# Kernel optimization log

Measured on AMD Instinct MI355X. Metric: run time of the kernel, lower is better.

The kernel has to match this reference:

```python
import jax, jax.numpy as jnp
import numpy as np

D_MODEL = 1024
N_HEADS = 16
D_K = D_MODEL // N_HEADS
D_FF = 4096
B, S = 2, 2048
LN_EPS = 1e-5
NEG_INF = -1e30  # finite stand-in for -inf; first (all-masked) row is overwritten by zeros anyway


def layer_norm(x, g, b):
    mu = jnp.mean(x, axis=-1, keepdims=True)
    var = jnp.mean(jnp.square(x - mu), axis=-1, keepdims=True)
    return (x - mu) * jax.lax.rsqrt(var + LN_EPS) * g + b


def setup_inputs() -> dict:
    key = jax.random.key(0)
    ks = jax.random.split(key, 16)
    sd = 0.02
    inp = {
        "query": jax.random.normal(ks[0], (B, S, D_MODEL), jnp.float32),
        "key": jax.random.normal(ks[1], (B, S, D_MODEL), jnp.float32),
        "values": jax.random.normal(ks[2], (B, S, D_MODEL), jnp.float32),
        "Wq": jax.random.normal(ks[3], (D_MODEL, D_MODEL), jnp.float32) * sd,
        "bq": jnp.zeros((D_MODEL,), jnp.float32),
        "Wk": jax.random.normal(ks[4], (D_MODEL, D_MODEL), jnp.float32) * sd,
        "bk": jnp.zeros((D_MODEL,), jnp.float32),
        "Wv": jax.random.normal(ks[5], (D_MODEL, D_MODEL), jnp.float32) * sd,
        "bv": jnp.zeros((D_MODEL,), jnp.float32),
        "Wo": jax.random.normal(ks[6], (D_MODEL, D_MODEL), jnp.float32) * sd,
        "bo": jnp.zeros((D_MODEL,), jnp.float32),
        "ln1_g": jnp.ones((D_MODEL,), jnp.float32),
        "ln1_b": jnp.zeros((D_MODEL,), jnp.float32),
        "W1": jax.random.normal(ks[7], (D_MODEL, D_FF), jnp.float32) * sd,
        "b1": jnp.zeros((D_FF,), jnp.float32),
        "W2": jax.random.normal(ks[8], (D_FF, D_MODEL), jnp.float32) * sd,
        "b2": jnp.zeros((D_MODEL,), jnp.float32),
        "ln2_g": jnp.ones((D_MODEL,), jnp.float32),
        "ln2_b": jnp.zeros((D_MODEL,), jnp.float32),
        "mask": 0,
    }
    return inp


def reference(query, key, values, Wq, bq, Wk, bk, Wv, bv, Wo, bo,
              ln1_g, ln1_b, W1, b1, W2, b2, ln2_g, ln2_b, mask):
    b, s, d = query.shape
    # projections -> [B, H, S, d_k]
    q = (query @ Wq + bq).reshape(b, s, N_HEADS, D_K).transpose(0, 2, 1, 3)
    k = (key @ Wk + bk).reshape(b, s, N_HEADS, D_K).transpose(0, 2, 1, 3)
    v = (values @ Wv + bv).reshape(b, s, N_HEADS, D_K).transpose(0, 2, 1, 3)
    # scores [B, H, S, S]
    scores = jnp.einsum("bhqd,bhkd->bhqk", q, k) / jnp.sqrt(jnp.float32(D_K))
    # torch: triu(ones, k=mask)==0 -> allowed iff j < i + mask
    i = jnp.arange(s)[:, None]
    j = jnp.arange(s)[None, :]
    allowed = j < (i + mask)
    scores = jnp.where(allowed, scores, NEG_INF)
    attn = jax.nn.softmax(scores, axis=-1)
    if mask == 0:
        # zero-pad trick: first query row (fully masked) is replaced by zeros
        attn = attn.at[:, :, 0, :].set(0.0)
    ctx = jnp.einsum("bhqk,bhkd->bhqd", attn, v)
    ctx = ctx.transpose(0, 2, 1, 3).reshape(b, s, d)
    attn_out = ctx @ Wo + bo
    x = layer_norm(query + attn_out, ln1_g, ln1_b)
    ffn = jax.nn.relu(x @ W1 + b1) @ W2 + b2
    out = layer_norm(x + ffn, ln2_g, ln2_b)
    return out
```

## Files before the change

### kernel.cpp

```cpp
#include <hip/hip_runtime.h>


typedef __attribute__((ext_vector_type(8))) __bf16 bf16x8;
typedef __attribute__((ext_vector_type(4))) float f32x4;

struct alignas(8)  S4 { short x, y, z, w; };
struct alignas(16) F4 { float x, y, z, w; };
struct alignas(16) I4 { int x, y, z, w; };

static __device__ __forceinline__ short f2bf(float f) {
  unsigned u = __float_as_uint(f);
  u += 0x7fff + ((u >> 16) & 1);
  return (short)(u >> 16);
}

static __device__ __forceinline__ void store_out(float* p, float v) { *p = v; }
static __device__ __forceinline__ void store_out(short* p, float v) { *p = f2bf(v); }

#define GLL16(g, l)                                                         \
  __builtin_amdgcn_global_load_lds(                                         \
      (__attribute__((address_space(1))) void*)(g),                         \
      (__attribute__((address_space(3))) void*)(l), 16, 0, 0)

__global__ __launch_bounds__(256) void cvt_bf16_kernel(
    const float* __restrict__ i0, const float* __restrict__ i1,
    const float* __restrict__ i2, short* __restrict__ o0,
    short* __restrict__ o1, short* __restrict__ o2) {
  int z = blockIdx.y;
  const float* in = z == 0 ? i0 : (z == 1 ? i1 : i2);
  short* out = z == 0 ? o0 : (z == 1 ? o1 : o2);
  int i = (blockIdx.x * 256 + threadIdx.x) * 4;
  F4 v = *(const F4*)(in + i);
  S4 o = { f2bf(v.x), f2bf(v.y), f2bf(v.z), f2bf(v.w) };
  *(S4*)(out + i) = o;
}

__global__ __launch_bounds__(256) void transpose_cvt_kernel(
    const float* __restrict__ Wq, const float* __restrict__ Wk,
    const float* __restrict__ Wv, const float* __restrict__ Wo,
    const float* __restrict__ W1, const float* __restrict__ W2,
    short* __restrict__ Wqt, short* __restrict__ Wkt,
    short* __restrict__ Wvt, short* __restrict__ Wot,
    short* __restrict__ W1t, short* __restrict__ W2t) {
  __shared__ float tile[64][65];
  int bid = blockIdx.x;
  const float* W; short* Wt; int K, N, kx, ny;
  if (bid < 1024) {
    int w = bid >> 8, t = bid & 255;
    W = w == 0 ? Wq : (w == 1 ? Wk : (w == 2 ? Wv : Wo));
    Wt = w == 0 ? Wqt : (w == 1 ? Wkt : (w == 2 ? Wvt : Wot));
    K = 1024; N = 1024; kx = t & 15; ny = t >> 4;
  } else if (bid < 2048) {
    int t = bid - 1024;
    W = W1; Wt = W1t; K = 1024; N = 4096; kx = t & 15; ny = t >> 4;
  } else {
    int t = bid - 2048;
    W = W2; Wt = W2t; K = 4096; N = 1024; kx = t & 63; ny = t >> 6;
  }
  int k0 = kx * 64, n0 = ny * 64;
  int tid = threadIdx.x;
  int rr = tid >> 4, cc = (tid & 15) * 4;
#pragma unroll
  for (int p = 0; p < 4; ++p) {
    int row = p * 16 + rr;
    F4 v = *(const F4*)&W[(long)(k0 + row) * N + n0 + cc];
    tile[row][cc] = v.x; tile[row][cc + 1] = v.y;
    tile[row][cc + 2] = v.z; tile[row][cc + 3] = v.w;
  }
  __syncthreads();
#pragma unroll
  for (int p = 0; p < 4; ++p) {
    int rn = p * 16 + rr;
    S4 o = { f2bf(tile[cc + 0][rn]), f2bf(tile[cc + 1][rn]),
             f2bf(tile[cc + 2][rn]), f2bf(tile[cc + 3][rn]) };
    *(S4*)&Wt[(long)(n0 + rn) * K + k0 + cc] = o;
  }
}

template <int OUT_MODE, bool RELU, bool RES, typename OT>
__device__ __forceinline__ void gemm_core(
    const short* __restrict__ A, const short* __restrict__ Bt,
    const float* __restrict__ bias, const float* __restrict__ res,
    OT* __restrict__ out, int M, int N, int K) {
  __shared__ __align__(16) short sA[128 * 64];
  __shared__ __align__(16) short sB[128 * 64];
  int tid = threadIdx.x;
  int lane = tid & 63, wave = tid >> 6;
  int col = lane & 15, quad = lane >> 4;
  int m0 = blockIdx.x * 128, n0 = blockIdx.y * 128;
  int wm = (wave & 1) * 64, wn = (wave >> 1) * 64;

  f32x4 acc[4][4] = {};

  for (int k0 = 0; k0 < K; k0 += 64) {
    __syncthreads();
#pragma unroll
    for (int j = 0; j < 4; ++j) {
      int idx = j * 256 + tid;
      int row = idx >> 3, cp = idx & 7;
      int c = cp ^ (row & 7);
      const short* ga = A  + (long)(m0 + row) * K + k0 + c * 8;
      const short* gb = Bt + (long)(n0 + row) * K + k0 + c * 8;
      short* la = &sA[(j * 256 + (wave << 6)) * 8];
      short* lb = &sB[(j * 256 + (wave << 6)) * 8];
      GLL16(ga, la);
      GLL16(gb, lb);
    }
    __syncthreads();

#pragma unroll
    for (int kk = 0; kk < 2; ++kk) {
      bf16x8 a[4], b[4];
#pragma unroll
      for (int t = 0; t < 4; ++t) {
        int ra = wm + t * 16 + col;
        int ca = kk * 4 + quad;
        a[t] = *(const bf16x8*)&sA[ra * 64 + ((ca ^ (ra & 7)) << 3)];
        int rb = wn + t * 16 + col;
        b[t] = *(const bf16x8*)&sB[rb * 64 + ((ca ^ (rb & 7)) << 3)];
      }
#pragma unroll
      for (int t = 0; t < 4; ++t)
#pragma unroll
        for (int u = 0; u < 4; ++u)
          acc[t][u] = __builtin_amdgcn_mfma_f32_16x16x32_bf16(
              a[t], b[u], acc[t][u], 0, 0, 0);
    }
  }

#pragma unroll
  for (int t = 0; t < 4; ++t) {
#pragma unroll
    for (int u = 0; u < 4; ++u) {
      int Cc = n0 + wn + u * 16 + col;
      float bv = bias[Cc];
#pragma unroll
      for (int r = 0; r < 4; ++r) {
        int R = m0 + wm + t * 16 + quad * 4 + r;
        float v = acc[t][u][r] + bv;
        if (RES) v += res[(long)R * N + Cc];
        if (RELU) v = v > 0.f ? v : 0.f;
        if (OUT_MODE == 0) {
          store_out(&out[(long)R * N + Cc], v);
        } else {
          int bb = R >> 11, s = R & 2047, h = Cc >> 6, d = Cc & 63;
          store_out(&out[((long)((bb * 16 + h) * 2048 + s) << 6) + d], v);
        }
      }
    }
  }
}

template <int OUT_MODE, bool RELU, bool RES, typename OT>
__global__ __launch_bounds__(256) void gemm_bt(
    const short* __restrict__ A, const short* __restrict__ Bt,
    const float* __restrict__ bias, const float* __restrict__ res,
    OT* __restrict__ out, int M, int N, int K) {
  gemm_core<OUT_MODE, RELU, RES, OT>(A, Bt, bias, res, out, M, N, K);
}

__global__ __launch_bounds__(256) void gemm_qkv(
    const short* __restrict__ Aq, const short* __restrict__ Ak,
    const short* __restrict__ Av, const short* __restrict__ Btq,
    const short* __restrict__ Btk, const short* __restrict__ Btv,
    const float* __restrict__ bq, const float* __restrict__ bk,
    const float* __restrict__ bv, short* __restrict__ Qp,
    short* __restrict__ Kp, short* __restrict__ Vp) {
  int z = blockIdx.z;
  const short* A = z == 0 ? Aq : (z == 1 ? Ak : Av);
  const short* Bt = z == 0 ? Btq : (z == 1 ? Btk : Btv);
  const float* bias = z == 0 ? bq : (z == 1 ? bk : bv);
  short* out = z == 0 ? Qp : (z == 1 ? Kp : Vp);
  gemm_core<1, false, false, short>(A, Bt, bias, nullptr, out, 4096, 1024, 1024);
}

__global__ __launch_bounds__(256) void attn_kernel(
    const short* __restrict__ Q, const short* __restrict__ K,
    const short* __restrict__ V, const int* __restrict__ maskp,
    short* __restrict__ ctx) {
  __shared__ __align__(16) short sK[2][64 * 64];
  __shared__ __align__(16) int   sVt[2][64 * 32];
  __shared__ __align__(16) short sP[4 * 16 * 64];
  int tid = threadIdx.x, lane = tid & 63, wave = tid >> 6;
  int col = lane & 15, quad = lane >> 4;
  int pair = blockIdx.x, bh = blockIdx.y;
  int maskv = maskp[0];
  const long base = (long)bh * (2048 * 64);
  int b = bh >> 4, h = bh & 15;

  int kp = tid & 31, dg = tid >> 5, d0v = dg * 8;

  for (int pass = 0; pass < 2; ++pass) {
    int qt = pass ? (31 - pair) : pair;
    int i0 = qt * 64 + wave * 16;

    long jmax = (long)qt * 64 + 63 + maskv - 1;
    int tot = (jmax < 0) ? 0 : (int)(jmax >> 6) + 1;
    if (tot > 32) tot = 32;

    bf16x8 aQ[2];
#pragma unroll
    for (int kk = 0; kk < 2; ++kk)
      aQ[kk] = *(const bf16x8*)&Q[base + (long)(i0 + col) * 64 + kk * 32 + quad * 8];

    f32x4 o[4] = {};
    float lsum[4] = { 0.f, 0.f, 0.f, 0.f };

    if (tot > 0) {
#pragma unroll
      for (int j = 0; j < 2; ++j) {
        int idx = j * 256 + tid;
        int row = idx >> 3, cp = idx & 7;
        int c = cp ^ (row & 7);
        GLL16(K + base + (long)row * 64 + c * 8,
              &sK[0][(j * 256 + (wave << 6)) * 8]);
      }
      {
        union { I4 v; short s[8]; } u0, u1;
        u0.v = *(const I4*)&V[base + (long)(2 * kp) * 64 + d0v];
        u1.v = *(const I4*)&V[base + (long)(2 * kp + 1) * 64 + d0v];
#pragma unroll
        for (int j = 0; j < 8; ++j) {
          int d = d0v + j;
          int w = ((int)(unsigned short)u1.s[j] << 16) | (unsigned short)u0.s[j];
          sVt[0][d * 32 + ((((kp >> 2) ^ (d & 7)) << 2) | (kp & 3))] = w;
        }
      }
    }
    __syncthreads();

    for (int kt = 0; kt < tot; ++kt) {
      int cur = kt & 1, nxt = cur ^ 1;
      bool pf = (kt + 1 < tot);

      union { I4 v; short s[8]; } u0, u1;
      if (pf) {
#pragma unroll
        for (int j = 0; j < 2; ++j) {
          int idx = j * 256 + tid;
          int row = idx >> 3, cp = idx & 7;
          int c = cp ^ (row & 7);
          GLL16(K + base + (long)((kt + 1) * 64 + row) * 64 + c * 8,
                &sK[nxt][(j * 256 + (wave << 6)) * 8]);
        }
        u0.v = *(const I4*)&V[base + (long)((kt + 1) * 64 + 2 * kp) * 64 + d0v];
        u1.v = *(const I4*)&V[base + (long)((kt + 1) * 64 + 2 * kp + 1) * 64 + d0v];
      }

      f32x4 sc[4] = {};
#pragma unroll
      for (int kk = 0; kk < 2; ++kk) {
        int ca = kk * 4 + quad;
#pragma unroll
        for (int nt = 0; nt < 4; ++nt) {
          int rk = nt * 16 + col;
          bf16x8 bK = *(const bf16x8*)&sK[cur][rk * 64 + ((ca ^ (rk & 7)) << 3)];
          sc[nt] = __builtin_amdgcn_mfma_f32_16x16x32_bf16(aQ[kk], bK, sc[nt], 0, 0, 0);
        }
      }

      bool interior = (kt * 64 + 63) < (qt * 64 + maskv);
      if (interior) {
#pragma unroll
        for (int r = 0; r < 4; ++r) {
          int qr = quad * 4 + r;
#pragma unroll
          for (int nt = 0; nt < 4; ++nt) {
            float p = __expf(sc[nt][r] * 0.125f);
            lsum[r] += p;
            int k8 = nt * 2 + (col >> 3);
            sP[wave * 1024 + qr * 64 + (((k8 ^ (qr & 7)) << 3) | (col & 7))] =
                f2bf(p);
          }
        }
      } else {
#pragma unroll
        for (int r = 0; r < 4; ++r) {
          int i = i0 + quad * 4 + r;
          int qr = quad * 4 + r;
#pragma unroll
          for (int nt = 0; nt < 4; ++nt) {
            int j = kt * 64 + nt * 16 + col;
            float p = (j < i + maskv) ? __expf(sc[nt][r] * 0.125f) : 0.f;
            lsum[r] += p;
            int k8 = nt * 2 + (col >> 3);
            sP[wave * 1024 + qr * 64 + (((k8 ^ (qr & 7)) << 3) | (col & 7))] =
                f2bf(p);
          }
        }
      }

#pragma unroll
      for (int kk = 0; kk < 2; ++kk) {
        int ca = kk * 4 + quad;
        bf16x8 aP = *(const bf16x8*)&sP[wave * 1024 + col * 64 + ((ca ^ (col & 7)) << 3)];
#pragma unroll
        for (int dt = 0; dt < 4; ++dt) {
          int d = dt * 16 + col;
          bf16x8 bV = *(const bf16x8*)((const short*)sVt[cur] + d * 64 + ((ca ^ (d & 7)) << 3));
          o[dt] = __builtin_amdgcn_mfma_f32_16x16x32_bf16(aP, bV, o[dt], 0, 0, 0);
        }
      }

      if (pf) {
#pragma unroll
        for (int j = 0; j < 8; ++j) {
          int d = d0v + j;
          int w = ((int)(unsigned short)u1.s[j] << 16) | (unsigned short)u0.s[j];
          sVt[nxt][d * 32 + ((((kp >> 2) ^ (d & 7)) << 2) | (kp & 3))] = w;
        }
      }
      __syncthreads();
    }

#pragma unroll
    for (int r = 0; r < 4; ++r)
#pragma unroll
      for (int off = 1; off < 16; off <<= 1)
        lsum[r] += __shfl_xor(lsum[r], off);

#pragma unroll
    for (int r = 0; r < 4; ++r) {
      int i = i0 + quad * 4 + r;
      float inv = (lsum[r] > 0.f) ? 1.f / lsum[r] : 0.f;
      if (maskv == 0 && i == 0) inv = 0.f;
#pragma unroll
      for (int dt = 0; dt < 4; ++dt)
        ctx[(long)(b * 2048 + i) * 1024 + h * 64 + dt * 16 + col] =
            f2bf(o[dt][r] * inv);
    }
    __syncthreads();
  }
}

__global__ __launch_bounds__(256) void ln_kernel(
    const float* __restrict__ in, const float* __restrict__ g,
    const float* __restrict__ b, float* __restrict__ outf,
    short* __restrict__ outb) {
  int r = blockIdx.x, tid = threadIdx.x;
  int lane = tid & 63, wave = tid >> 6;
  F4 v = ((const F4*)(in + (long)r * 1024))[tid];
  float s = v.x + v.y + v.z + v.w;
  float sq = v.x * v.x + v.y * v.y + v.z * v.z + v.w * v.w;
#pragma unroll
  for (int off = 1; off < 64; off <<= 1) {
    s += __shfl_xor(s, off);
    sq += __shfl_xor(sq, off);
  }
  __shared__ float rs[4], rq[4];
  if (lane == 0) { rs[wave] = s; rq[wave] = sq; }
  __syncthreads();
  s = rs[0] + rs[1] + rs[2] + rs[3];
  sq = rq[0] + rq[1] + rq[2] + rq[3];
  float mu = s * (1.0f / 1024.0f);
  float var = sq * (1.0f / 1024.0f) - mu * mu;
  float rstd = rsqrtf(var + 1e-5f);
  F4 gv = ((const F4*)g)[tid], bv = ((const F4*)b)[tid];
  F4 o;
  o.x = (v.x - mu) * rstd * gv.x + bv.x;
  o.y = (v.y - mu) * rstd * gv.y + bv.y;
  o.z = (v.z - mu) * rstd * gv.z + bv.z;
  o.w = (v.w - mu) * rstd * gv.w + bv.w;
  ((F4*)(outf + (long)r * 1024))[tid] = o;
  if (outb) {
    S4 ob = { f2bf(o.x), f2bf(o.y), f2bf(o.z), f2bf(o.w) };
    ((S4*)(outb + (long)r * 1024))[tid] = ob;
  }
}

extern "C" void kernel_launch(void* const* d_in, const int* in_sizes, int n_in,
                              void* d_out, int out_size, void* d_ws, size_t ws_size,
                              hipStream_t stream) {
  const float* query  = (const float*)d_in[0];
  const float* keyi   = (const float*)d_in[1];
  const float* values = (const float*)d_in[2];
  const float* Wq = (const float*)d_in[3];
  const float* bq = (const float*)d_in[4];
  const float* Wk = (const float*)d_in[5];
  const float* bk = (const float*)d_in[6];
  const float* Wv = (const float*)d_in[7];
  const float* bv = (const float*)d_in[8];
  const float* Wo = (const float*)d_in[9];
  const float* bo = (const float*)d_in[10];
  const float* ln1_g = (const float*)d_in[11];
  const float* ln1_b = (const float*)d_in[12];
  const float* W1 = (const float*)d_in[13];
  const float* b1 = (const float*)d_in[14];
  const float* W2 = (const float*)d_in[15];
  const float* b2 = (const float*)d_in[16];
  const float* ln2_g = (const float*)d_in[17];
  const float* ln2_b = (const float*)d_in[18];
  const int*   maskp = (const int*)d_in[19];
  float* out = (float*)d_out;

  char* ws = (char*)d_ws;
  const size_t MB = 1u << 20;
  short* q_bf = (short*)(ws + 0);
  short* k_bf = (short*)(ws + 8 * MB);
  short* v_bf = (short*)(ws + 16 * MB);
  short* ctx  = (short*)(ws + 24 * MB);
  short* Qp   = (short*)(ws + 32 * MB);
  short* Kp   = (short*)(ws + 40 * MB);
  short* Vp   = (short*)(ws + 48 * MB);
  float* attn_res = (float*)(ws + 0);
  float* ffn_res  = (float*)(ws + 16 * MB);
  float* x_f32    = (float*)(ws + 32 * MB);
  short* x_bf     = (short*)(ws + 48 * MB);
  short* Wqt = (short*)(ws + 56 * MB);
  short* Wkt = (short*)(ws + 58 * MB);
  short* Wvt = (short*)(ws + 60 * MB);
  short* Wot = (short*)(ws + 62 * MB);
  short* W1t = (short*)(ws + 64 * MB);
  short* W2t = (short*)(ws + 72 * MB);
  short* hbuf = (short*)(ws + 80 * MB);

  cvt_bf16_kernel<<<dim3(4096, 3), 256, 0, stream>>>(query, keyi, values,
                                                     q_bf, k_bf, v_bf);
  transpose_cvt_kernel<<<3072, 256, 0, stream>>>(Wq, Wk, Wv, Wo, W1, W2,
                                                 Wqt, Wkt, Wvt, Wot, W1t, W2t);
  gemm_qkv<<<dim3(32, 8, 3), 256, 0, stream>>>(q_bf, k_bf, v_bf,
                                               Wqt, Wkt, Wvt,
                                               bq, bk, bv, Qp, Kp, Vp);
  attn_kernel<<<dim3(16, 32), 256, 0, stream>>>(Qp, Kp, Vp, maskp, ctx);
  gemm_bt<0, false, true, float><<<dim3(32, 8), 256, 0, stream>>>(
      ctx, Wot, bo, query, attn_res, 4096, 1024, 1024);
  ln_kernel<<<4096, 256, 0, stream>>>(attn_res, ln1_g, ln1_b, x_f32, x_bf);
  gemm_bt<0, true, false, short><<<dim3(32, 32), 256, 0, stream>>>(
      x_bf, W1t, b1, nullptr, hbuf, 4096, 4096, 1024);
  gemm_bt<0, false, true, float><<<dim3(32, 8), 256, 0, stream>>>(
      hbuf, W2t, b2, x_f32, ffn_res, 4096, 1024, 4096);
  ln_kernel<<<4096, 256, 0, stream>>>(ffn_res, ln2_g, ln2_b, out, nullptr);

  (void)in_sizes; (void)n_in; (void)out_size; (void)ws_size;
}
```

Before: 422.9 us.

## Split-K the N=1024 GEMMs and fold partial sums into LayerNorm

The Wo and W2 projections, whose output is 4096x1024, now run as two-way split-K GEMMs. Each half writes fp32 partials to its own buffer, which doubles the grid from 256 to 512 blocks so the many compute units on the chip are better occupied. The residual add moves out of the GEMM epilogue into a new LayerNorm kernel that sums both partials plus the residual before normalising. The cost is extra fp32 partial traffic to and from memory, and each split block has half as many K iterations to amortise its epilogue.

```diff
diff --git a/kernel.cpp b/kernel.cpp
--- a/kernel.cpp
+++ b/kernel.cpp
@@ -81,7 +81,7 @@
 __device__ __forceinline__ void gemm_core(
     const short* __restrict__ A, const short* __restrict__ Bt,
     const float* __restrict__ bias, const float* __restrict__ res,
-    OT* __restrict__ out, int M, int N, int K) {
+    OT* __restrict__ out, int M, int N, int K, int kBeg, int kEnd) {
   __shared__ __align__(16) short sA[128 * 64];
   __shared__ __align__(16) short sB[128 * 64];
   int tid = threadIdx.x;
@@ -92,7 +92,7 @@
 
   f32x4 acc[4][4] = {};
 
-  for (int k0 = 0; k0 < K; k0 += 64) {
+  for (int k0 = kBeg; k0 < kEnd; k0 += 64) {
     __syncthreads();
 #pragma unroll
     for (int j = 0; j < 4; ++j) {
@@ -133,7 +133,7 @@
 #pragma unroll
     for (int u = 0; u < 4; ++u) {
       int Cc = n0 + wn + u * 16 + col;
-      float bv = bias[Cc];
+      float bv = bias ? bias[Cc] : 0.f;
 #pragma unroll
       for (int r = 0; r < 4; ++r) {
         int R = m0 + wm + t * 16 + quad * 4 + r;
@@ -156,7 +156,19 @@
     const short* __restrict__ A, const short* __restrict__ Bt,
     const float* __restrict__ bias, const float* __restrict__ res,
     OT* __restrict__ out, int M, int N, int K) {
-  gemm_core<OUT_MODE, RELU, RES, OT>(A, Bt, bias, res, out, M, N, K);
+  gemm_core<OUT_MODE, RELU, RES, OT>(A, Bt, bias, res, out, M, N, K, 0, K);
+}
+
+__global__ __launch_bounds__(256) void gemm_splitk(
+    const short* __restrict__ A, const short* __restrict__ Bt,
+    const float* __restrict__ bias, float* __restrict__ p0,
+    float* __restrict__ p1, int M, int N, int K) {
+  int z = blockIdx.z;
+  float* out = z == 0 ? p0 : p1;
+  const float* b = z == 0 ? bias : nullptr;
+  int kc = K >> 1;
+  gemm_core<0, false, false, float>(A, Bt, b, nullptr, out, M, N, K,
+                                    z * kc, z * kc + kc);
 }
 
 __global__ __launch_bounds__(256) void gemm_qkv(
@@ -171,7 +183,8 @@
   const short* Bt = z == 0 ? Btq : (z == 1 ? Btk : Btv);
   const float* bias = z == 0 ? bq : (z == 1 ? bk : bv);
   short* out = z == 0 ? Qp : (z == 1 ? Kp : Vp);
-  gemm_core<1, false, false, short>(A, Bt, bias, nullptr, out, 4096, 1024, 1024);
+  gemm_core<1, false, false, short>(A, Bt, bias, nullptr, out,
+                                    4096, 1024, 1024, 0, 1024);
 }
 
 __global__ __launch_bounds__(256) void attn_kernel(
@@ -333,13 +346,18 @@
   }
 }
 
-__global__ __launch_bounds__(256) void ln_kernel(
-    const float* __restrict__ in, const float* __restrict__ g,
+__global__ __launch_bounds__(256) void ln_comb_kernel(
+    const float* __restrict__ p0, const float* __restrict__ p1,
+    const float* __restrict__ res, const float* __restrict__ g,
     const float* __restrict__ b, float* __restrict__ outf,
     short* __restrict__ outb) {
   int r = blockIdx.x, tid = threadIdx.x;
   int lane = tid & 63, wave = tid >> 6;
-  F4 v = ((const F4*)(in + (long)r * 1024))[tid];
+  long off0 = (long)r * 1024;
+  F4 a = ((const F4*)(p0 + off0))[tid];
+  F4 c = ((const F4*)(p1 + off0))[tid];
+  F4 d = ((const F4*)(res + off0))[tid];
+  F4 v = { a.x + c.x + d.x, a.y + c.y + d.y, a.z + c.z + d.z, a.w + c.w + d.w };
   float s = v.x + v.y + v.z + v.w;
   float sq = v.x * v.x + v.y * v.y + v.z * v.z + v.w * v.w;
 #pragma unroll
@@ -361,10 +379,10 @@
   o.y = (v.y - mu) * rstd * gv.y + bv.y;
   o.z = (v.z - mu) * rstd * gv.z + bv.z;
   o.w = (v.w - mu) * rstd * gv.w + bv.w;
-  ((F4*)(outf + (long)r * 1024))[tid] = o;
+  ((F4*)(outf + off0))[tid] = o;
   if (outb) {
     S4 ob = { f2bf(o.x), f2bf(o.y), f2bf(o.z), f2bf(o.w) };
-    ((S4*)(outb + (long)r * 1024))[tid] = ob;
+    ((S4*)(outb + off0))[tid] = ob;
   }
 }
 
@@ -402,17 +420,19 @@
   short* Qp   = (short*)(ws + 32 * MB);
   short* Kp   = (short*)(ws + 40 * MB);
   short* Vp   = (short*)(ws + 48 * MB);
-  float* attn_res = (float*)(ws + 0);
-  float* ffn_res  = (float*)(ws + 16 * MB);
-  float* x_f32    = (float*)(ws + 32 * MB);
-  short* x_bf     = (short*)(ws + 48 * MB);
-  short* Wqt = (short*)(ws + 56 * MB);
-  short* Wkt = (short*)(ws + 58 * MB);
-  short* Wvt = (short*)(ws + 60 * MB);
-  short* Wot = (short*)(ws + 62 * MB);
-  short* W1t = (short*)(ws + 64 * MB);
-  short* W2t = (short*)(ws + 72 * MB);
+  short* Wqt  = (short*)(ws + 56 * MB);
+  short* Wkt  = (short*)(ws + 58 * MB);
+  short* Wvt  = (short*)(ws + 60 * MB);
+  short* Wot  = (short*)(ws + 62 * MB);
+  short* W1t  = (short*)(ws + 64 * MB);
+  short* W2t  = (short*)(ws + 72 * MB);
   short* hbuf = (short*)(ws + 80 * MB);
+  float* pWo0 = (float*)(ws + 0);
+  float* pWo1 = (float*)(ws + 32 * MB);
+  float* x_f32 = (float*)(ws + 16 * MB);
+  short* x_bf  = (short*)(ws + 48 * MB);
+  float* pF0 = (float*)(ws + 0);
+  float* pF1 = (float*)(ws + 32 * MB);
 
   cvt_bf16_kernel<<<dim3(4096, 3), 256, 0, stream>>>(query, keyi, values,
                                                      q_bf, k_bf, v_bf);
@@ -422,14 +442,16 @@
                                                Wqt, Wkt, Wvt,
                                                bq, bk, bv, Qp, Kp, Vp);
   attn_kernel<<<dim3(16, 32), 256, 0, stream>>>(Qp, Kp, Vp, maskp, ctx);
-  gemm_bt<0, false, true, float><<<dim3(32, 8), 256, 0, stream>>>(
-      ctx, Wot, bo, query, attn_res, 4096, 1024, 1024);
-  ln_kernel<<<4096, 256, 0, stream>>>(attn_res, ln1_g, ln1_b, x_f32, x_bf);
+  gemm_splitk<<<dim3(32, 8, 2), 256, 0, stream>>>(ctx, Wot, bo, pWo0, pWo1,
+                                                  4096, 1024, 1024);
+  ln_comb_kernel<<<4096, 256, 0, stream>>>(pWo0, pWo1, query, ln1_g, ln1_b,
+                                           x_f32, x_bf);
   gemm_bt<0, true, false, short><<<dim3(32, 32), 256, 0, stream>>>(
       x_bf, W1t, b1, nullptr, hbuf, 4096, 4096, 1024);
-  gemm_bt<0, false, true, float><<<dim3(32, 8), 256, 0, stream>>>(
-      hbuf, W2t, b2, x_f32, ffn_res, 4096, 1024, 4096);
-  ln_kernel<<<4096, 256, 0, stream>>>(ffn_res, ln2_g, ln2_b, out, nullptr);
+  gemm_splitk<<<dim3(32, 8, 2), 256, 0, stream>>>(hbuf, W2t, b2, pF0, pF1,
+                                                  4096, 1024, 4096);
+  ln_comb_kernel<<<4096, 256, 0, stream>>>(pF0, pF1, x_f32, ln2_g, ln2_b,
+                                           out, nullptr);
 
   (void)in_sizes; (void)n_in; (void)out_size; (void)ws_size;
 }
```

Result: faster. 412.2 us (-2.5%).
